# Optimization experiments

Measured on AMD Instinct MI355X. Metric: run time of the kernel, lower is better.

## Reference

```python
import jax, jax.numpy as jnp
import numpy as np

D_MODEL, N_EXPERTS, N_VIEWS, N_TOKENS = 256, 16, 3, 8192

def setup_inputs() -> dict:
    key = jax.random.key(0)
    ks = jax.random.split(key, 10)
    s = 0.05
    return {
        "v0": jax.random.normal(ks[0], (N_TOKENS, D_MODEL), jnp.float32),
        "v1": jax.random.normal(ks[1], (N_TOKENS, D_MODEL), jnp.float32),
        "v2": jax.random.normal(ks[2], (N_TOKENS, D_MODEL), jnp.float32),
        "router_w": jax.random.normal(ks[3], (N_VIEWS, N_EXPERTS, D_MODEL), jnp.float32) * s,
        "expert_keys": jax.random.normal(ks[4], (N_EXPERTS, D_MODEL), jnp.float32) * s,
        "W1": jax.random.normal(ks[5], (N_EXPERTS, D_MODEL, 4 * D_MODEL), jnp.float32) * s,
        "b1": jax.random.normal(ks[6], (N_EXPERTS, 4 * D_MODEL), jnp.float32) * s,
        "W2": jax.random.normal(ks[7], (N_EXPERTS, 4 * D_MODEL, D_MODEL), jnp.float32) * s,
        "b2": jax.random.normal(ks[8], (N_EXPERTS, D_MODEL), jnp.float32) * s,
        "top_k": 4,
    }

def _laplace_gate(v, rw, expert_keys, top_k):
    # -||v - key||^2 expanded: -(|v|^2 + |k|^2 - 2 v.k)   -> [N, E]
    sq = (jnp.sum(v * v, -1, keepdims=True)
          + jnp.sum(expert_keys * expert_keys, -1)[None, :]
          - 2.0 * (v @ expert_keys.T))
    logits = -sq + v @ rw.T                      # router(h), no bias
    topv, topi = jax.lax.top_k(logits, top_k)    # [N, K]
    gate = jax.nn.softmax(topv, axis=-1)         # exp(topv - logsumexp(topv))
    return gate, topi

def reference(v0, v1, v2, router_w, expert_keys, W1, b1, W2, b2, top_k):
    views = [v0, v1, v2]
    E = expert_keys.shape[0]
    N = v0.shape[0]
    fused = jnp.zeros_like(v0)
    rows = jnp.arange(N)[:, None]
    for i, v in enumerate(views):
        gate, idx = _laplace_gate(v, router_w[i], expert_keys, top_k)
        # scatter top-k gates into a dense [N, E] combine matrix
        dense_gate = jnp.zeros((N, E), v.dtype).at[rows, idx].add(gate)
        out = jnp.zeros_like(v)
        for e in range(E):  # fixed small expert loop; each token combined via its gate
            h = jax.nn.gelu(v @ W1[e] + b1[e], approximate=False)
            out = out + dense_gate[:, e:e + 1] * (h @ W2[e] + b2[e])
        fused = fused + out
    return fused
```

## Files before the change

### kernel.cpp

```cpp
#include <hip/hip_runtime.h>
#include <math.h>

#define D_MODEL 256
#define N_EXP   16
#define N_VIEWS 3
#define N_TOK   8192
#define TOPK    4
#define HDIM    1024
#define CH      64
#define NCH     16
#define ROWS    64
#define NGROUP  48
#define NT_STRIPE 2048
#define NT_SPILL  1600
#define NT_TOTAL  (NT_STRIPE + NT_SPILL)
#define REC_ELTS 32768

typedef short s16x8 __attribute__((ext_vector_type(8)));
typedef float f32x4 __attribute__((ext_vector_type(4)));

__device__ __forceinline__ unsigned short f2bf(float x) {
    union { float f; unsigned u; } a; a.f = x;
    unsigned r = a.u + 0x7FFFu + ((a.u >> 16) & 1u);
    return (unsigned short)(r >> 16);
}

__device__ __forceinline__ void dma16(const unsigned short* gp, unsigned short* lp) {
    __builtin_amdgcn_global_load_lds(
        (const __attribute__((address_space(1))) unsigned int*)gp,
        (__attribute__((address_space(3))) unsigned int*)lp, 16, 0, 0);
}

__device__ __forceinline__ void dma_half(const unsigned short* gsrc, unsigned short* ldst,
                                         int wave, int lane) {
    #pragma unroll
    for (int i = 0; i < 4; i++) {
        int blk = wave * 4 + i;
        dma16(gsrc + ((size_t)blk * 64 + lane) * 8, ldst + blk * 512);
    }
}

__global__ __launch_bounds__(256) void wfrag_kernel(const float* __restrict__ W1,
                                                    const float* __restrict__ W2,
                                                    unsigned short* __restrict__ Wf) {
    int c = blockIdx.x, e = blockIdx.y;
    unsigned short* dst = Wf + (size_t)(e * NCH + c) * REC_ELTS;
    if (blockIdx.z == 0) {
        const float* src = W1 + (size_t)e * 256 * 1024;
        #pragma unroll
        for (int i = 0; i < 8; i++) {
            int idx = threadIdx.x + i * 256;
            int lane = idx & 63, nt = (idx >> 6) & 3, ks = idx >> 8;
            int ncol = c * 64 + nt * 16 + (lane & 15);
            int kbase = ks * 32 + (lane >> 4) * 8;
            s16x8 o;
            #pragma unroll
            for (int j = 0; j < 8; j++) o[j] = (short)f2bf(src[(size_t)(kbase + j) * 1024 + ncol]);
            *(s16x8*)(dst + (size_t)idx * 8) = o;
        }
    } else {
        const float* src = W2 + (size_t)e * 1024 * 256;
        dst += 16384;
        #pragma unroll
        for (int i = 0; i < 8; i++) {
            int idx = threadIdx.x + i * 256;
            int lane = idx & 63, ntile = (idx >> 6) & 15, ks2 = idx >> 10;
            int n = ntile * 16 + (lane & 15);
            int kbase = c * 64 + ks2 * 32 + (lane >> 4) * 8;
            s16x8 o;
            #pragma unroll
            for (int j = 0; j < 8; j++) o[j] = (short)f2bf(src[(size_t)(kbase + j) * 256 + n]);
            *(s16x8*)(dst + (size_t)idx * 8) = o;
        }
    }
}

__global__ __launch_bounds__(256) void route_kernel(
    const float* __restrict__ v0, const float* __restrict__ v1, const float* __restrict__ v2,
    const float* __restrict__ rw, const float* __restrict__ keys,
    unsigned short* __restrict__ Xbf,
    int* __restrict__ gidx, float* __restrict__ ggate, int* __restrict__ counts)
{
    __shared__ __align__(16) float cwS[N_EXP * D_MODEL];
    __shared__ float knS[N_EXP];
    __shared__ int lcnt[N_EXP];
    int view = blockIdx.y;
    const float* src = view == 0 ? v0 : (view == 1 ? v1 : v2);
    for (int i = threadIdx.x; i < N_EXP * D_MODEL; i += 256)
        cwS[i] = rw[view * N_EXP * D_MODEL + i] + 2.0f * keys[i];
    if (threadIdx.x < N_EXP) {
        const float4* kp = (const float4*)(keys + threadIdx.x * D_MODEL);
        float s = 0.f;
        for (int d = 0; d < 64; d++) { float4 k = kp[d]; s += k.x*k.x + k.y*k.y + k.z*k.z + k.w*k.w; }
        knS[threadIdx.x] = s; lcnt[threadIdx.x] = 0;
    }
    __syncthreads();

    int wave = threadIdx.x >> 6, lane = threadIdx.x & 63;
    for (int t = 0; t < 16; t++) {
        int token = blockIdx.x * 64 + wave * 16 + t;
        float4 v = ((const float4*)(src + (size_t)token * D_MODEL))[lane];
        ushort4 xo; xo.x = f2bf(v.x); xo.y = f2bf(v.y); xo.z = f2bf(v.z); xo.w = f2bf(v.w);
        ((ushort4*)(Xbf + ((size_t)view * N_TOK + token) * D_MODEL))[lane] = xo;
        float lg[N_EXP];
        #pragma unroll
        for (int e = 0; e < N_EXP; e++) {
            float4 w = *(const float4*)&cwS[e * D_MODEL + lane * 4];
            float p = v.x * w.x + v.y * w.y + v.z * w.z + v.w * w.w;
            #pragma unroll
            for (int s = 32; s > 0; s >>= 1) p += __shfl_xor(p, s, 64);
            lg[e] = p - knS[e];
        }
        int idxs[TOPK]; float vals[TOPK];
        #pragma unroll
        for (int k = 0; k < TOPK; k++) {
            float best = -1e30f; int bi = 0;
            #pragma unroll
            for (int e = 0; e < N_EXP; e++)
                if (lg[e] > best) { best = lg[e]; bi = e; }
            idxs[k] = bi; vals[k] = best;
            #pragma unroll
            for (int e = 0; e < N_EXP; e++)
                lg[e] = (e == bi) ? -1e30f : lg[e];
        }
        float m = vals[0], s = 0.f, ex[TOPK];
        #pragma unroll
        for (int k = 0; k < TOPK; k++) { ex[k] = __expf(vals[k] - m); s += ex[k]; }
        float inv = 1.0f / s;
        if (lane == 0) {
            size_t t4 = ((size_t)view * N_TOK + token) * TOPK;
            int4 gi; gi.x = idxs[0]; gi.y = idxs[1]; gi.z = idxs[2]; gi.w = idxs[3];
            *(int4*)&gidx[t4] = gi;
            float4 gv; gv.x = ex[0]*inv; gv.y = ex[1]*inv; gv.z = ex[2]*inv; gv.w = ex[3]*inv;
            *(float4*)&ggate[t4] = gv;
            atomicAdd(&lcnt[idxs[0]], 1); atomicAdd(&lcnt[idxs[1]], 1);
            atomicAdd(&lcnt[idxs[2]], 1); atomicAdd(&lcnt[idxs[3]], 1);
        }
    }
    __syncthreads();
    if (threadIdx.x < N_EXP && lcnt[threadIdx.x])
        atomicAdd(&counts[view * N_EXP + threadIdx.x], lcnt[threadIdx.x]);
}

__global__ void scan_kernel(const int* __restrict__ counts, int* __restrict__ offs,
                            int* __restrict__ cursor, int* __restrict__ tiles,
                            int* __restrict__ spillCnt) {
    __shared__ int ntS[NGROUP];
    int t = threadIdx.x;
    if (t == 0) spillCnt[0] = 0;
    if (t < NGROUP) ntS[t] = (counts[t] + ROWS - 1) / ROWS;
    for (int s = t; s < NT_TOTAL; s += 64) tiles[s] = -1;
    __syncthreads();
    if (t <= NGROUP) {
        int acc = 0;
        for (int g = 0; g < t && g < NGROUP; g++) acc += counts[g];
        if (t < NGROUP) { offs[t] = acc; cursor[t] = acc; }
        else offs[NGROUP] = acc;
    }
    if (t < NGROUP) {
        int x = (t & 15) >> 1;
        int kstart = 0;
        for (int g2 = 0; g2 < t; g2++)
            if (((g2 & 15) >> 1) == x) kstart += ntS[g2];
        int nt = ntS[t];
        for (int i = 0; i < nt; i++) {
            int k = kstart + i, rec = (t << 16) | i;
            if (k < NT_STRIPE / 8) tiles[x + 8 * k] = rec;
            else {
                int sp = atomicAdd(spillCnt, 1);
                if (sp < NT_SPILL) tiles[NT_STRIPE + sp] = rec;
            }
        }
    }
}

__global__ __launch_bounds__(256) void fill_kernel(const int* __restrict__ gidx,
                                                   const float* __restrict__ ggate,
                                                   int* __restrict__ cursor,
                                                   int* __restrict__ rowTok,
                                                   float* __restrict__ rowGate) {
    __shared__ int lc[N_EXP], lbase[N_EXP];
    int view = blockIdx.y;
    int token = blockIdx.x * 256 + threadIdx.x;
    if (threadIdx.x < N_EXP) lc[threadIdx.x] = 0;
    __syncthreads();
    size_t t4 = ((size_t)view * N_TOK + token) * TOPK;
    int4 e4 = *(const int4*)&gidx[t4];
    float4 g4 = *(const float4*)&ggate[t4];
    int e[4] = { e4.x, e4.y, e4.z, e4.w };
    float gg[4] = { g4.x, g4.y, g4.z, g4.w };
    int lp[4];
    #pragma unroll
    for (int k = 0; k < TOPK; k++) lp[k] = atomicAdd(&lc[e[k]], 1);
    __syncthreads();
    if (threadIdx.x < N_EXP)
        lbase[threadIdx.x] = lc[threadIdx.x] ? atomicAdd(&cursor[view * N_EXP + threadIdx.x], lc[threadIdx.x]) : 0;
    __syncthreads();
    #pragma unroll
    for (int k = 0; k < TOPK; k++) {
        int pos = lbase[e[k]] + lp[k];
        rowTok[pos] = token;
        rowGate[pos] = gg[k];
    }
}

__global__ __launch_bounds__(512, 4) void ffn_kernel(
    const unsigned short* __restrict__ Xbf, const unsigned short* __restrict__ Wf,
    const float* __restrict__ b1, const float* __restrict__ b2,
    const int* __restrict__ offs, const int* __restrict__ tiles,
    const int* __restrict__ rowTok, const float* __restrict__ rowGate,
    float* __restrict__ out)
{
    __shared__ __align__(16) unsigned short Wbuf[REC_ELTS];
    __shared__ __align__(16) unsigned short Hc[ROWS * CH];
    __shared__ int   tokS[ROWS];
    __shared__ float gateS[ROWS];

    int rec = tiles[blockIdx.x];
    if (rec < 0) return;
    int g = rec >> 16, view = g >> 4, e = g & 15;
    int base = offs[g];
    int L = offs[g + 1] - base;
    int r0 = (rec & 0xffff) * ROWS;

    int tid = threadIdx.x;
    int wave = tid >> 6, lane = tid & 63, lmod = lane & 15, quad = lane >> 4;

    const unsigned short* wchunk = Wf + (size_t)e * NCH * REC_ELTS;
    dma_half(wchunk, Wbuf, wave, lane);

    if (tid < ROWS) {
        int gr = r0 + tid; bool ok = gr < L;
        tokS[tid]  = ok ? rowTok[base + gr] : -1;
        gateS[tid] = ok ? rowGate[base + gr] : 0.f;
    }

    int mt1 = wave & 3, nh = wave >> 2;
    int ms  = wave & 1, ns = wave >> 1;

    __syncthreads();

    s16x8 areg[8];
    {
        int token = tokS[mt1 * 16 + lmod];
        if (token < 0) token = 0;
        const unsigned short* xp = Xbf + ((size_t)view * N_TOK + token) * D_MODEL;
        #pragma unroll
        for (int ks = 0; ks < 8; ks++)
            areg[ks] = *(const s16x8*)(xp + ks * 32 + quad * 8);
    }
    dma_half(wchunk + 16384, Wbuf + 16384, wave, lane);

    f32x4 acc2[2][4];
    #pragma unroll
    for (int i = 0; i < 2; i++)
        #pragma unroll
        for (int j = 0; j < 4; j++) acc2[i][j] = (f32x4){0.f, 0.f, 0.f, 0.f};

    for (int c = 0; c < NCH; c++) {
        f32x4 acc1[2];
        acc1[0] = (f32x4){0.f, 0.f, 0.f, 0.f};
        acc1[1] = (f32x4){0.f, 0.f, 0.f, 0.f};
        #pragma unroll
        for (int ks = 0; ks < 8; ks++) {
            #pragma unroll
            for (int nt = 0; nt < 2; nt++) {
                s16x8 b = *(const s16x8*)&Wbuf[((ks * 4 + nh * 2 + nt) * 64 + lane) * 8];
                acc1[nt] = __builtin_amdgcn_mfma_f32_16x16x32_bf16(areg[ks], b, acc1[nt], 0, 0, 0);
            }
        }
        #pragma unroll
        for (int nt = 0; nt < 2; nt++) {
            float bb = b1[e * HDIM + c * CH + (nh * 2 + nt) * 16 + lmod];
            int qa = nt * 2 + (lmod >> 3);
            int baseo = ((mt1 * 2 + nh) * 64 + qa * 16 + quad * 4) * 8 + (lmod & 7);
            #pragma unroll
            for (int r = 0; r < 4; r++) {
                float h = acc1[nt][r] + bb;
                float u = h * (0.7978845608f + 0.0356774081f * h * h);
                float ex2 = __expf(2.f * u);
                float tn = 1.f - 2.f * __builtin_amdgcn_rcpf(1.f + ex2);
                Hc[baseo + r * 8] = f2bf(0.5f * h * (1.f + tn));
            }
        }
        __syncthreads();
        if (c < NCH - 1)
            dma_half(wchunk + (size_t)(c + 1) * REC_ELTS, Wbuf, wave, lane);
        #pragma unroll
        for (int ks2 = 0; ks2 < 2; ks2++) {
            s16x8 afr[2];
            #pragma unroll
            for (int mt = 0; mt < 2; mt++)
                afr[mt] = *(const s16x8*)&Hc[(((ms * 2 + mt) * 2 + ks2) * 64 + lane) * 8];
            #pragma unroll
            for (int nt = 0; nt < 4; nt++) {
                s16x8 b = *(const s16x8*)&Wbuf[16384 + ((ks2 * 16 + ns * 4 + nt) * 64 + lane) * 8];
                #pragma unroll
                for (int mt = 0; mt < 2; mt++)
                    acc2[mt][nt] = __builtin_amdgcn_mfma_f32_16x16x32_bf16(
                        afr[mt], b, acc2[mt][nt], 0, 0, 0);
            }
        }
        __syncthreads();
        if (c < NCH - 1)
            dma_half(wchunk + (size_t)(c + 1) * REC_ELTS + 16384, Wbuf + 16384, wave, lane);
    }

    #pragma unroll
    for (int nt = 0; nt < 4; nt++) {
        int col = (ns * 4 + nt) * 16 + lmod;
        float b2v = b2[e * D_MODEL + col];
        #pragma unroll
        for (int mt = 0; mt < 2; mt++) {
            #pragma unroll
            for (int r = 0; r < 4; r++) {
                int rloc = (ms * 2 + mt) * 16 + quad * 4 + r;
                if (r0 + rloc < L) {
                    atomicAdd(&out[(size_t)tokS[rloc] * D_MODEL + col],
                              gateS[rloc] * (acc2[mt][nt][r] + b2v));
                }
            }
        }
    }
}

extern "C" void kernel_launch(void* const* d_in, const int* in_sizes, int n_in,
                              void* d_out, int out_size, void* d_ws, size_t ws_size,
                              hipStream_t stream)
{
    const float* v0   = (const float*)d_in[0];
    const float* v1   = (const float*)d_in[1];
    const float* v2   = (const float*)d_in[2];
    const float* rw   = (const float*)d_in[3];
    const float* keys = (const float*)d_in[4];
    const float* W1   = (const float*)d_in[5];
    const float* b1   = (const float*)d_in[6];
    const float* W2   = (const float*)d_in[7];
    const float* b2   = (const float*)d_in[8];
    float* out = (float*)d_out;

    char* p = (char*)d_ws;
    unsigned short* Xbf = (unsigned short*)p; p += (size_t)N_VIEWS * N_TOK * D_MODEL * 2;
    unsigned short* Wf  = (unsigned short*)p; p += (size_t)N_EXP * NCH * REC_ELTS * 2;
    int*   counts = (int*)p;   p += 256;
    int*   offs   = (int*)p;   p += 256;
    int*   cursor = (int*)p;   p += 256;
    int*   spill  = (int*)p;   p += 256;
    int*   tiles  = (int*)p;   p += NT_TOTAL * 4 + 64;
    int*   gidx   = (int*)p;   p += (size_t)N_VIEWS * N_TOK * TOPK * 4;
    float* ggate  = (float*)p; p += (size_t)N_VIEWS * N_TOK * TOPK * 4;
    int*   rowTok = (int*)p;   p += (size_t)N_VIEWS * N_TOK * TOPK * 4;
    float* rowGate= (float*)p; p += (size_t)N_VIEWS * N_TOK * TOPK * 4;

    hipMemsetAsync(counts, 0, NGROUP * sizeof(int), stream);
    hipMemsetAsync(out, 0, (size_t)out_size * sizeof(float), stream);

    wfrag_kernel<<<dim3(NCH, N_EXP, 2), 256, 0, stream>>>(W1, W2, Wf);
    route_kernel<<<dim3(N_TOK / 64, N_VIEWS), 256, 0, stream>>>(v0, v1, v2, rw, keys, Xbf,
                                                                gidx, ggate, counts);
    scan_kernel<<<1, 64, 0, stream>>>(counts, offs, cursor, tiles, spill);
    fill_kernel<<<dim3(N_TOK / 256, N_VIEWS), 256, 0, stream>>>(gidx, ggate, cursor,
                                                                rowTok, rowGate);
    ffn_kernel<<<dim3(NT_TOTAL), 512, 0, stream>>>(Xbf, Wf, b1, b2, offs, tiles,
                                                   rowTok, rowGate, out);
}
```

Measured before the change: 393.6 us.

## Warp-specialize FFN into GEMM1/GEMM2 wave groups with 32x32 MFMA and double-buffered H

Splits the FFN block's eight waves into two groups: four waves compute the first GEMM plus GELU for chunk c, while the other four run the second GEMM on chunk c-1 from a double-buffered H tile. Both GEMMs switch from 16x16x32 to 32x32x16 bf16 MFMA, and the weight fragment layout in wfrag_kernel is rewritten to match. The X operand and the output accumulator share one register array, and the spill tile count is reduced. The aim is to overlap the two GEMM phases and cut LDS fragment traffic per MFMA, at the cost of half the waves per phase and higher register pressure.

Measured after the change: 439.4 us. +11.6%, slower.

```diff
diff --git a/kernel.cpp b/kernel.cpp
--- a/kernel.cpp
+++ b/kernel.cpp
@@ -12,12 +12,13 @@
 #define ROWS    64
 #define NGROUP  48
 #define NT_STRIPE 2048
-#define NT_SPILL  1600
+#define NT_SPILL  512
 #define NT_TOTAL  (NT_STRIPE + NT_SPILL)
 #define REC_ELTS 32768
 
 typedef short s16x8 __attribute__((ext_vector_type(8)));
 typedef float f32x4 __attribute__((ext_vector_type(4)));
+typedef float f32x16 __attribute__((ext_vector_type(16)));
 
 __device__ __forceinline__ unsigned short f2bf(float x) {
     union { float f; unsigned u; } a; a.f = x;
@@ -50,9 +51,9 @@
         #pragma unroll
         for (int i = 0; i < 8; i++) {
             int idx = threadIdx.x + i * 256;
-            int lane = idx & 63, nt = (idx >> 6) & 3, ks = idx >> 8;
-            int ncol = c * 64 + nt * 16 + (lane & 15);
-            int kbase = ks * 32 + (lane >> 4) * 8;
+            int lane = idx & 63, nh = (idx >> 6) & 1, kt = idx >> 7;
+            int ncol = c * 64 + nh * 32 + (lane & 31);
+            int kbase = kt * 16 + (lane >> 5) * 8;
             s16x8 o;
             #pragma unroll
             for (int j = 0; j < 8; j++) o[j] = (short)f2bf(src[(size_t)(kbase + j) * 1024 + ncol]);
@@ -64,9 +65,9 @@
         #pragma unroll
         for (int i = 0; i < 8; i++) {
             int idx = threadIdx.x + i * 256;
-            int lane = idx & 63, ntile = (idx >> 6) & 15, ks2 = idx >> 10;
-            int n = ntile * 16 + (lane & 15);
-            int kbase = c * 64 + ks2 * 32 + (lane >> 4) * 8;
+            int lane = idx & 63, nt = (idx >> 6) & 7, kt2 = idx >> 9;
+            int n = nt * 32 + (lane & 31);
+            int kbase = c * 64 + kt2 * 16 + (lane >> 5) * 8;
             s16x8 o;
             #pragma unroll
             for (int j = 0; j < 8; j++) o[j] = (short)f2bf(src[(size_t)(kbase + j) * 256 + n]);
@@ -211,10 +212,9 @@
     const int* __restrict__ rowTok, const float* __restrict__ rowGate,
     float* __restrict__ out)
 {
-    __shared__ __align__(16) unsigned short Wbuf[REC_ELTS];
-    __shared__ __align__(16) unsigned short Hc[ROWS * CH];
-    __shared__ int   tokS[ROWS];
-    __shared__ float gateS[ROWS];
+    __shared__ __align__(16) unsigned short W1s[16384];
+    __shared__ __align__(16) unsigned short W2s[16384];
+    __shared__ __align__(16) unsigned short HcS[2][4096];
 
     int rec = tiles[blockIdx.x];
     if (rec < 0) return;
@@ -224,100 +224,104 @@
     int r0 = (rec & 0xffff) * ROWS;
 
     int tid = threadIdx.x;
-    int wave = tid >> 6, lane = tid & 63, lmod = lane & 15, quad = lane >> 4;
+    int wave = tid >> 6, lane = tid & 63;
+    bool isG1 = wave < 4;
+    int mt = wave & 1, nh = (wave >> 1) & 1;
+    int u = wave & 3, ms = u & 1, ng = u >> 1;
 
     const unsigned short* wchunk = Wf + (size_t)e * NCH * REC_ELTS;
-    dma_half(wchunk, Wbuf, wave, lane);
-
-    if (tid < ROWS) {
-        int gr = r0 + tid; bool ok = gr < L;
-        tokS[tid]  = ok ? rowTok[base + gr] : -1;
-        gateS[tid] = ok ? rowGate[base + gr] : 0.f;
-    }
-
-    int mt1 = wave & 3, nh = wave >> 2;
-    int ms  = wave & 1, ns = wave >> 1;
-
-    __syncthreads();
-
-    s16x8 areg[8];
-    {
-        int token = tokS[mt1 * 16 + lmod];
-        if (token < 0) token = 0;
+    dma_half(wchunk, W1s, wave, lane);
+
+    f32x16 zz;
+    #pragma unroll
+    for (int i = 0; i < 16; i++) zz[i] = 0.f;
+
+    f32x16 st[4];
+    if (isG1) {
+        int gr = r0 + mt * 32 + (lane & 31);
+        int token = (gr < L) ? rowTok[base + gr] : 0;
         const unsigned short* xp = Xbf + ((size_t)view * N_TOK + token) * D_MODEL;
-        #pragma unroll
-        for (int ks = 0; ks < 8; ks++)
-            areg[ks] = *(const s16x8*)(xp + ks * 32 + quad * 8);
-    }
-    dma_half(wchunk + 16384, Wbuf + 16384, wave, lane);
-
-    f32x4 acc2[2][4];
-    #pragma unroll
-    for (int i = 0; i < 2; i++)
-        #pragma unroll
-        for (int j = 0; j < 4; j++) acc2[i][j] = (f32x4){0.f, 0.f, 0.f, 0.f};
-
-    for (int c = 0; c < NCH; c++) {
-        f32x4 acc1[2];
-        acc1[0] = (f32x4){0.f, 0.f, 0.f, 0.f};
-        acc1[1] = (f32x4){0.f, 0.f, 0.f, 0.f};
-        #pragma unroll
-        for (int ks = 0; ks < 8; ks++) {
-            #pragma unroll
-            for (int nt = 0; nt < 2; nt++) {
-                s16x8 b = *(const s16x8*)&Wbuf[((ks * 4 + nh * 2 + nt) * 64 + lane) * 8];
-                acc1[nt] = __builtin_amdgcn_mfma_f32_16x16x32_bf16(areg[ks], b, acc1[nt], 0, 0, 0);
+        int h = lane >> 5;
+        #pragma unroll
+        for (int kt = 0; kt < 16; kt++) {
+            float4 x = *(const float4*)(xp + kt * 16 + h * 8);
+            st[kt >> 2][(kt & 3) * 4 + 0] = x.x;
+            st[kt >> 2][(kt & 3) * 4 + 1] = x.y;
+            st[kt >> 2][(kt & 3) * 4 + 2] = x.z;
+            st[kt >> 2][(kt & 3) * 4 + 3] = x.w;
+        }
+    } else {
+        #pragma unroll
+        for (int i = 0; i < 4; i++) st[i] = zz;
+    }
+    __syncthreads();
+
+    for (int c = 0; c <= NCH; c++) {
+        if (isG1) {
+            if (c < NCH) {
+                f32x16 a0 = zz, a1 = zz;
+                #pragma unroll
+                for (int kt = 0; kt < 16; kt += 2) {
+                    float4 t0 = { st[kt >> 2][(kt & 3) * 4], st[kt >> 2][(kt & 3) * 4 + 1],
+                                  st[kt >> 2][(kt & 3) * 4 + 2], st[kt >> 2][(kt & 3) * 4 + 3] };
+                    s16x8 af0 = __builtin_bit_cast(s16x8, t0);
+                    s16x8 b0 = *(const s16x8*)&W1s[((kt * 2 + nh) * 64 + lane) * 8];
+                    a0 = __builtin_amdgcn_mfma_f32_32x32x16_bf16(af0, b0, a0, 0, 0, 0);
+                    int k1 = kt + 1;
+                    float4 t1 = { st[k1 >> 2][(k1 & 3) * 4], st[k1 >> 2][(k1 & 3) * 4 + 1],
+                                  st[k1 >> 2][(k1 & 3) * 4 + 2], st[k1 >> 2][(k1 & 3) * 4 + 3] };
+                    s16x8 af1 = __builtin_bit_cast(s16x8, t1);
+                    s16x8 b1f = *(const s16x8*)&W1s[((k1 * 2 + nh) * 64 + lane) * 8];
+                    a1 = __builtin_amdgcn_mfma_f32_32x32x16_bf16(af1, b1f, a1, 0, 0, 0);
+                }
+                float bb = b1[e * HDIM + c * CH + nh * 32 + (lane & 31)];
+                unsigned short* hdst = &HcS[c & 1][((mt * 2 + nh) * 16) * 64 + lane];
+                #pragma unroll
+                for (int r = 0; r < 16; r++) {
+                    float hv = a0[r] + a1[r] + bb;
+                    float uu = hv * (0.7978845608f + 0.0356774081f * hv * hv);
+                    float ex2 = __expf(2.f * uu);
+                    float tn = 1.f - 2.f * __builtin_amdgcn_rcpf(1.f + ex2);
+                    hdst[r * 64] = f2bf(0.5f * hv * (1.f + tn));
+                }
             }
-        }
-        #pragma unroll
-        for (int nt = 0; nt < 2; nt++) {
-            float bb = b1[e * HDIM + c * CH + (nh * 2 + nt) * 16 + lmod];
-            int qa = nt * 2 + (lmod >> 3);
-            int baseo = ((mt1 * 2 + nh) * 64 + qa * 16 + quad * 4) * 8 + (lmod & 7);
-            #pragma unroll
-            for (int r = 0; r < 4; r++) {
-                float h = acc1[nt][r] + bb;
-                float u = h * (0.7978845608f + 0.0356774081f * h * h);
-                float ex2 = __expf(2.f * u);
-                float tn = 1.f - 2.f * __builtin_amdgcn_rcpf(1.f + ex2);
-                Hc[baseo + r * 8] = f2bf(0.5f * h * (1.f + tn));
+        } else {
+            if (c > 0) {
+                int row = lane & 31, h = lane >> 5;
+                int r_ = (row & 3) + 4 * (row >> 3);
+                int w5 = (row >> 2) & 1;
+                const unsigned short* hsrc = &HcS[(c - 1) & 1][0];
+                #pragma unroll
+                for (int kt2 = 0; kt2 < 4; kt2++) {
+                    s16x8 a = *(const s16x8*)&hsrc[((ms * 2 + (kt2 >> 1)) * 16 + r_) * 64
+                                                   + w5 * 32 + (kt2 & 1) * 16 + h * 8];
+                    #pragma unroll
+                    for (int nt = 0; nt < 4; nt++) {
+                        s16x8 b = *(const s16x8*)&W2s[((kt2 * 8 + ng * 4 + nt) * 64 + lane) * 8];
+                        st[nt] = __builtin_amdgcn_mfma_f32_32x32x16_bf16(a, b, st[nt], 0, 0, 0);
+                    }
+                }
             }
         }
         __syncthreads();
-        if (c < NCH - 1)
-            dma_half(wchunk + (size_t)(c + 1) * REC_ELTS, Wbuf, wave, lane);
-        #pragma unroll
-        for (int ks2 = 0; ks2 < 2; ks2++) {
-            s16x8 afr[2];
-            #pragma unroll
-            for (int mt = 0; mt < 2; mt++)
-                afr[mt] = *(const s16x8*)&Hc[(((ms * 2 + mt) * 2 + ks2) * 64 + lane) * 8];
-            #pragma unroll
-            for (int nt = 0; nt < 4; nt++) {
-                s16x8 b = *(const s16x8*)&Wbuf[16384 + ((ks2 * 16 + ns * 4 + nt) * 64 + lane) * 8];
-                #pragma unroll
-                for (int mt = 0; mt < 2; mt++)
-                    acc2[mt][nt] = __builtin_amdgcn_mfma_f32_16x16x32_bf16(
-                        afr[mt], b, acc2[mt][nt], 0, 0, 0);
-            }
-        }
+        if (c + 1 < NCH) dma_half(wchunk + (size_t)(c + 1) * REC_ELTS, W1s, wave, lane);
+        if (c < NCH)     dma_half(wchunk + (size_t)c * REC_ELTS + 16384, W2s, wave, lane);
         __syncthreads();
-        if (c < NCH - 1)
-            dma_half(wchunk + (size_t)(c + 1) * REC_ELTS + 16384, Wbuf + 16384, wave, lane);
-    }
-
-    #pragma unroll
-    for (int nt = 0; nt < 4; nt++) {
-        int col = (ns * 4 + nt) * 16 + lmod;
-        float b2v = b2[e * D_MODEL + col];
-        #pragma unroll
-        for (int mt = 0; mt < 2; mt++) {
-            #pragma unroll
-            for (int r = 0; r < 4; r++) {
-                int rloc = (ms * 2 + mt) * 16 + quad * 4 + r;
-                if (r0 + rloc < L) {
-                    atomicAdd(&out[(size_t)tokS[rloc] * D_MODEL + col],
-                              gateS[rloc] * (acc2[mt][nt][r] + b2v));
+    }
+
+    if (!isG1) {
+        #pragma unroll
+        for (int nt = 0; nt < 4; nt++) {
+            int col = (ng * 4 + nt) * 32 + (lane & 31);
+            float b2v = b2[e * D_MODEL + col];
+            #pragma unroll
+            for (int r = 0; r < 16; r++) {
+                int rloc = ms * 32 + (r & 3) + 8 * (r >> 2) + 4 * (lane >> 5);
+                int gr = r0 + rloc;
+                if (gr < L) {
+                    int token = rowTok[base + gr];
+                    float gate = rowGate[base + gr];
+                    atomicAdd(&out[(size_t)token * D_MODEL + col], gate * (st[nt][r] + b2v));
                 }
             }
         }
```

## Merge weight prep with routing and remap FFN first-GEMM wave tiling

Applied to the files above, without the earlier changes.

Fuses the weight-fragment conversion and routing kernels into one launch of 896 blocks, so the two independent jobs can run concurrently and one launch is saved. In the FFN kernel, each wave now computes two M-tiles against a single N-tile, so every B fragment read from LDS feeds two MFMAs. This halves LDS traffic for the first GEMM at the cost of more A registers. The spill tile count is also cut from 1600 to 512, which shrinks the grid but risks dropping tiles if the spill capacity is ever exceeded.

Result: slower. 416.0 us (+5.7%).

```diff
diff --git a/kernel.cpp b/kernel.cpp
--- a/kernel.cpp
+++ b/kernel.cpp
@@ -12,7 +12,7 @@
 #define ROWS    64
 #define NGROUP  48
 #define NT_STRIPE 2048
-#define NT_SPILL  1600
+#define NT_SPILL  512
 #define NT_TOTAL  (NT_STRIPE + NT_SPILL)
 #define REC_ELTS 32768
 
@@ -40,51 +40,54 @@
     }
 }
 
-__global__ __launch_bounds__(256) void wfrag_kernel(const float* __restrict__ W1,
-                                                    const float* __restrict__ W2,
-                                                    unsigned short* __restrict__ Wf) {
-    int c = blockIdx.x, e = blockIdx.y;
-    unsigned short* dst = Wf + (size_t)(e * NCH + c) * REC_ELTS;
-    if (blockIdx.z == 0) {
-        const float* src = W1 + (size_t)e * 256 * 1024;
-        #pragma unroll
-        for (int i = 0; i < 8; i++) {
-            int idx = threadIdx.x + i * 256;
-            int lane = idx & 63, nt = (idx >> 6) & 3, ks = idx >> 8;
-            int ncol = c * 64 + nt * 16 + (lane & 15);
-            int kbase = ks * 32 + (lane >> 4) * 8;
-            s16x8 o;
-            #pragma unroll
-            for (int j = 0; j < 8; j++) o[j] = (short)f2bf(src[(size_t)(kbase + j) * 1024 + ncol]);
-            *(s16x8*)(dst + (size_t)idx * 8) = o;
-        }
-    } else {
-        const float* src = W2 + (size_t)e * 1024 * 256;
-        dst += 16384;
-        #pragma unroll
-        for (int i = 0; i < 8; i++) {
-            int idx = threadIdx.x + i * 256;
-            int lane = idx & 63, ntile = (idx >> 6) & 15, ks2 = idx >> 10;
-            int n = ntile * 16 + (lane & 15);
-            int kbase = c * 64 + ks2 * 32 + (lane >> 4) * 8;
-            s16x8 o;
-            #pragma unroll
-            for (int j = 0; j < 8; j++) o[j] = (short)f2bf(src[(size_t)(kbase + j) * 256 + n]);
-            *(s16x8*)(dst + (size_t)idx * 8) = o;
-        }
-    }
-}
-
-__global__ __launch_bounds__(256) void route_kernel(
+__global__ __launch_bounds__(256) void prep_kernel(
     const float* __restrict__ v0, const float* __restrict__ v1, const float* __restrict__ v2,
     const float* __restrict__ rw, const float* __restrict__ keys,
-    unsigned short* __restrict__ Xbf,
+    const float* __restrict__ W1, const float* __restrict__ W2,
+    unsigned short* __restrict__ Wf, unsigned short* __restrict__ Xbf,
     int* __restrict__ gidx, float* __restrict__ ggate, int* __restrict__ counts)
 {
     __shared__ __align__(16) float cwS[N_EXP * D_MODEL];
     __shared__ float knS[N_EXP];
     __shared__ int lcnt[N_EXP];
-    int view = blockIdx.y;
+
+    int bid = blockIdx.x;
+    if (bid < 512) {
+        int c = bid & 15, e = (bid >> 4) & 15, z = bid >> 8;
+        unsigned short* dst = Wf + (size_t)(e * NCH + c) * REC_ELTS;
+        if (z == 0) {
+            const float* src = W1 + (size_t)e * 256 * 1024;
+            #pragma unroll
+            for (int i = 0; i < 8; i++) {
+                int idx = threadIdx.x + i * 256;
+                int lane = idx & 63, nt = (idx >> 6) & 3, ks = idx >> 8;
+                int ncol = c * 64 + nt * 16 + (lane & 15);
+                int kbase = ks * 32 + (lane >> 4) * 8;
+                s16x8 o;
+                #pragma unroll
+                for (int j = 0; j < 8; j++) o[j] = (short)f2bf(src[(size_t)(kbase + j) * 1024 + ncol]);
+                *(s16x8*)(dst + (size_t)idx * 8) = o;
+            }
+        } else {
+            const float* src = W2 + (size_t)e * 1024 * 256;
+            dst += 16384;
+            #pragma unroll
+            for (int i = 0; i < 8; i++) {
+                int idx = threadIdx.x + i * 256;
+                int lane = idx & 63, ntile = (idx >> 6) & 15, ks2 = idx >> 10;
+                int n = ntile * 16 + (lane & 15);
+                int kbase = c * 64 + ks2 * 32 + (lane >> 4) * 8;
+                s16x8 o;
+                #pragma unroll
+                for (int j = 0; j < 8; j++) o[j] = (short)f2bf(src[(size_t)(kbase + j) * 256 + n]);
+                *(s16x8*)(dst + (size_t)idx * 8) = o;
+            }
+        }
+        return;
+    }
+
+    int rb = bid - 512;
+    int view = rb >> 7, xb = rb & 127;
     const float* src = view == 0 ? v0 : (view == 1 ? v1 : v2);
     for (int i = threadIdx.x; i < N_EXP * D_MODEL; i += 256)
         cwS[i] = rw[view * N_EXP * D_MODEL + i] + 2.0f * keys[i];
@@ -98,7 +101,7 @@
 
     int wave = threadIdx.x >> 6, lane = threadIdx.x & 63;
     for (int t = 0; t < 16; t++) {
-        int token = blockIdx.x * 64 + wave * 16 + t;
+        int token = xb * 64 + wave * 16 + t;
         float4 v = ((const float4*)(src + (size_t)token * D_MODEL))[lane];
         ushort4 xo; xo.x = f2bf(v.x); xo.y = f2bf(v.y); xo.z = f2bf(v.z); xo.w = f2bf(v.w);
         ((ushort4*)(Xbf + ((size_t)view * N_TOK + token) * D_MODEL))[lane] = xo;
@@ -235,19 +238,20 @@
         gateS[tid] = ok ? rowGate[base + gr] : 0.f;
     }
 
-    int mt1 = wave & 3, nh = wave >> 2;
-    int ms  = wave & 1, ns = wave >> 1;
-
-    __syncthreads();
-
-    s16x8 areg[8];
-    {
-        int token = tokS[mt1 * 16 + lmod];
+    int mh  = wave & 1, nt1 = wave >> 1;
+    int ms  = wave & 1, ns  = wave >> 1;
+
+    __syncthreads();
+
+    s16x8 areg[2][8];
+    #pragma unroll
+    for (int mt2 = 0; mt2 < 2; mt2++) {
+        int token = tokS[(mh * 2 + mt2) * 16 + lmod];
         if (token < 0) token = 0;
         const unsigned short* xp = Xbf + ((size_t)view * N_TOK + token) * D_MODEL;
         #pragma unroll
         for (int ks = 0; ks < 8; ks++)
-            areg[ks] = *(const s16x8*)(xp + ks * 32 + quad * 8);
+            areg[mt2][ks] = *(const s16x8*)(xp + ks * 32 + quad * 8);
     }
     dma_half(wchunk + 16384, Wbuf + 16384, wave, lane);
 
@@ -263,24 +267,25 @@
         acc1[1] = (f32x4){0.f, 0.f, 0.f, 0.f};
         #pragma unroll
         for (int ks = 0; ks < 8; ks++) {
-            #pragma unroll
-            for (int nt = 0; nt < 2; nt++) {
-                s16x8 b = *(const s16x8*)&Wbuf[((ks * 4 + nh * 2 + nt) * 64 + lane) * 8];
-                acc1[nt] = __builtin_amdgcn_mfma_f32_16x16x32_bf16(areg[ks], b, acc1[nt], 0, 0, 0);
-            }
-        }
-        #pragma unroll
-        for (int nt = 0; nt < 2; nt++) {
-            float bb = b1[e * HDIM + c * CH + (nh * 2 + nt) * 16 + lmod];
-            int qa = nt * 2 + (lmod >> 3);
-            int baseo = ((mt1 * 2 + nh) * 64 + qa * 16 + quad * 4) * 8 + (lmod & 7);
-            #pragma unroll
-            for (int r = 0; r < 4; r++) {
-                float h = acc1[nt][r] + bb;
-                float u = h * (0.7978845608f + 0.0356774081f * h * h);
-                float ex2 = __expf(2.f * u);
-                float tn = 1.f - 2.f * __builtin_amdgcn_rcpf(1.f + ex2);
-                Hc[baseo + r * 8] = f2bf(0.5f * h * (1.f + tn));
+            s16x8 b = *(const s16x8*)&Wbuf[((ks * 4 + nt1) * 64 + lane) * 8];
+            acc1[0] = __builtin_amdgcn_mfma_f32_16x16x32_bf16(areg[0][ks], b, acc1[0], 0, 0, 0);
+            acc1[1] = __builtin_amdgcn_mfma_f32_16x16x32_bf16(areg[1][ks], b, acc1[1], 0, 0, 0);
+        }
+        {
+            float bb = b1[e * HDIM + c * CH + nt1 * 16 + lmod];
+            int kh = nt1 >> 1;
+            int qa = (nt1 & 1) * 2 + (lmod >> 3);
+            #pragma unroll
+            for (int mt2 = 0; mt2 < 2; mt2++) {
+                int baseo = (((mh * 2 + mt2) * 2 + kh) * 64 + qa * 16 + quad * 4) * 8 + (lmod & 7);
+                #pragma unroll
+                for (int r = 0; r < 4; r++) {
+                    float h = acc1[mt2][r] + bb;
+                    float u = h * (0.7978845608f + 0.0356774081f * h * h);
+                    float ex2 = __expf(2.f * u);
+                    float tn = 1.f - 2.f * __builtin_amdgcn_rcpf(1.f + ex2);
+                    Hc[baseo + r * 8] = f2bf(0.5f * h * (1.f + tn));
+                }
             }
         }
         __syncthreads();
@@ -355,9 +360,8 @@
     hipMemsetAsync(counts, 0, NGROUP * sizeof(int), stream);
     hipMemsetAsync(out, 0, (size_t)out_size * sizeof(float), stream);
 
-    wfrag_kernel<<<dim3(NCH, N_EXP, 2), 256, 0, stream>>>(W1, W2, Wf);
-    route_kernel<<<dim3(N_TOK / 64, N_VIEWS), 256, 0, stream>>>(v0, v1, v2, rw, keys, Xbf,
-                                                                gidx, ggate, counts);
+    prep_kernel<<<896, 256, 0, stream>>>(v0, v1, v2, rw, keys, W1, W2,
+                                         Wf, Xbf, gidx, ggate, counts);
     scan_kernel<<<1, 64, 0, stream>>>(counts, offs, cursor, tiles, spill);
     fill_kernel<<<dim3(N_TOK / 256, N_VIEWS), 256, 0, stream>>>(gidx, ggate, cursor,
                                                                 rowTok, rowGate);
```

## Merge weight repacking and routing into one prep kernel with LDS transpose

Applied to the files above, without the earlier changes.

Combines the weight bf16 fragment repacking and the routing kernel into one launch. The first 512 blocks handle the weights and the remaining 384 blocks do routing. The weight repack now reads W1/W2 with coalesced float4 loads into a padded shared-memory tile and transposes from there, replacing strided scalar global reads. It also cuts the spill tile count, which reduces the number of empty FFN blocks launched but risks overflow if spill demand is high.

After: 391.5 us. Within noise of the previous version (-0.5%).

```diff
diff --git a/kernel.cpp b/kernel.cpp
--- a/kernel.cpp
+++ b/kernel.cpp
@@ -12,7 +12,7 @@
 #define ROWS    64
 #define NGROUP  48
 #define NT_STRIPE 2048
-#define NT_SPILL  1600
+#define NT_SPILL  512
 #define NT_TOTAL  (NT_STRIPE + NT_SPILL)
 #define REC_ELTS 32768
 
@@ -40,65 +40,95 @@
     }
 }
 
-__global__ __launch_bounds__(256) void wfrag_kernel(const float* __restrict__ W1,
-                                                    const float* __restrict__ W2,
-                                                    unsigned short* __restrict__ Wf) {
-    int c = blockIdx.x, e = blockIdx.y;
-    unsigned short* dst = Wf + (size_t)(e * NCH + c) * REC_ELTS;
-    if (blockIdx.z == 0) {
-        const float* src = W1 + (size_t)e * 256 * 1024;
-        #pragma unroll
-        for (int i = 0; i < 8; i++) {
-            int idx = threadIdx.x + i * 256;
-            int lane = idx & 63, nt = (idx >> 6) & 3, ks = idx >> 8;
-            int ncol = c * 64 + nt * 16 + (lane & 15);
-            int kbase = ks * 32 + (lane >> 4) * 8;
-            s16x8 o;
-            #pragma unroll
-            for (int j = 0; j < 8; j++) o[j] = (short)f2bf(src[(size_t)(kbase + j) * 1024 + ncol]);
-            *(s16x8*)(dst + (size_t)idx * 8) = o;
-        }
-    } else {
-        const float* src = W2 + (size_t)e * 1024 * 256;
-        dst += 16384;
-        #pragma unroll
-        for (int i = 0; i < 8; i++) {
-            int idx = threadIdx.x + i * 256;
-            int lane = idx & 63, ntile = (idx >> 6) & 15, ks2 = idx >> 10;
-            int n = ntile * 16 + (lane & 15);
-            int kbase = c * 64 + ks2 * 32 + (lane >> 4) * 8;
-            s16x8 o;
-            #pragma unroll
-            for (int j = 0; j < 8; j++) o[j] = (short)f2bf(src[(size_t)(kbase + j) * 256 + n]);
-            *(s16x8*)(dst + (size_t)idx * 8) = o;
-        }
-    }
-}
-
-__global__ __launch_bounds__(256) void route_kernel(
+#define T1_STRIDE 65
+#define T2_STRIDE 257
+
+__global__ __launch_bounds__(256) void prep_kernel(
     const float* __restrict__ v0, const float* __restrict__ v1, const float* __restrict__ v2,
     const float* __restrict__ rw, const float* __restrict__ keys,
-    unsigned short* __restrict__ Xbf,
+    const float* __restrict__ W1, const float* __restrict__ W2,
+    unsigned short* __restrict__ Wf, unsigned short* __restrict__ Xbf,
     int* __restrict__ gidx, float* __restrict__ ggate, int* __restrict__ counts)
 {
-    __shared__ __align__(16) float cwS[N_EXP * D_MODEL];
-    __shared__ float knS[N_EXP];
-    __shared__ int lcnt[N_EXP];
-    int view = blockIdx.y;
+    __shared__ __align__(16) char smem[256 * T1_STRIDE * 4];
+
+    int bid = blockIdx.x;
+    int tid = threadIdx.x;
+    if (bid < 512) {
+        int c = bid & 15, e = (bid >> 4) & 15, z = bid >> 8;
+        unsigned short* dst = Wf + (size_t)(e * NCH + c) * REC_ELTS;
+        if (z == 0) {
+            float* T1 = (float*)smem;
+            const float* src = W1 + (size_t)e * 256 * 1024 + c * 64;
+            #pragma unroll
+            for (int p = 0; p < 16; p++) {
+                int k = p * 16 + (tid >> 4), c4 = (tid & 15) * 4;
+                float4 v = *(const float4*)(src + (size_t)k * 1024 + c4);
+                T1[k * T1_STRIDE + c4]     = v.x;
+                T1[k * T1_STRIDE + c4 + 1] = v.y;
+                T1[k * T1_STRIDE + c4 + 2] = v.z;
+                T1[k * T1_STRIDE + c4 + 3] = v.w;
+            }
+            __syncthreads();
+            #pragma unroll
+            for (int i = 0; i < 8; i++) {
+                int idx = tid + i * 256;
+                int lane = idx & 63, nt = (idx >> 6) & 3, ks = idx >> 8;
+                int nl = nt * 16 + (lane & 15);
+                int kbase = ks * 32 + (lane >> 4) * 8;
+                s16x8 o;
+                #pragma unroll
+                for (int j = 0; j < 8; j++) o[j] = (short)f2bf(T1[(kbase + j) * T1_STRIDE + nl]);
+                *(s16x8*)(dst + (size_t)idx * 8) = o;
+            }
+        } else {
+            float* T2 = (float*)smem;
+            const float* src = W2 + ((size_t)e * 1024 + c * 64) * 256;
+            #pragma unroll
+            for (int p = 0; p < 16; p++) {
+                int k2l = p * 4 + (tid >> 6), c4 = (tid & 63) * 4;
+                float4 v = *(const float4*)(src + (size_t)k2l * 256 + c4);
+                T2[k2l * T2_STRIDE + c4]     = v.x;
+                T2[k2l * T2_STRIDE + c4 + 1] = v.y;
+                T2[k2l * T2_STRIDE + c4 + 2] = v.z;
+                T2[k2l * T2_STRIDE + c4 + 3] = v.w;
+            }
+            __syncthreads();
+            dst += 16384;
+            #pragma unroll
+            for (int i = 0; i < 8; i++) {
+                int idx = tid + i * 256;
+                int lane = idx & 63, ntile = (idx >> 6) & 15, ks2 = idx >> 10;
+                int n = ntile * 16 + (lane & 15);
+                int kbase = ks2 * 32 + (lane >> 4) * 8;
+                s16x8 o;
+                #pragma unroll
+                for (int j = 0; j < 8; j++) o[j] = (short)f2bf(T2[(kbase + j) * T2_STRIDE + n]);
+                *(s16x8*)(dst + (size_t)idx * 8) = o;
+            }
+        }
+        return;
+    }
+
+    float* cwS = (float*)smem;
+    float* knS = (float*)(smem + 16384);
+    int*  lcnt = (int*)(smem + 16384 + 64);
+    int rb = bid - 512;
+    int view = rb >> 7, xb = rb & 127;
     const float* src = view == 0 ? v0 : (view == 1 ? v1 : v2);
-    for (int i = threadIdx.x; i < N_EXP * D_MODEL; i += 256)
+    for (int i = tid; i < N_EXP * D_MODEL; i += 256)
         cwS[i] = rw[view * N_EXP * D_MODEL + i] + 2.0f * keys[i];
-    if (threadIdx.x < N_EXP) {
-        const float4* kp = (const float4*)(keys + threadIdx.x * D_MODEL);
+    if (tid < N_EXP) {
+        const float4* kp = (const float4*)(keys + tid * D_MODEL);
         float s = 0.f;
         for (int d = 0; d < 64; d++) { float4 k = kp[d]; s += k.x*k.x + k.y*k.y + k.z*k.z + k.w*k.w; }
-        knS[threadIdx.x] = s; lcnt[threadIdx.x] = 0;
-    }
-    __syncthreads();
-
-    int wave = threadIdx.x >> 6, lane = threadIdx.x & 63;
+        knS[tid] = s; lcnt[tid] = 0;
+    }
+    __syncthreads();
+
+    int wave = tid >> 6, lane = tid & 63;
     for (int t = 0; t < 16; t++) {
-        int token = blockIdx.x * 64 + wave * 16 + t;
+        int token = xb * 64 + wave * 16 + t;
         float4 v = ((const float4*)(src + (size_t)token * D_MODEL))[lane];
         ushort4 xo; xo.x = f2bf(v.x); xo.y = f2bf(v.y); xo.z = f2bf(v.z); xo.w = f2bf(v.w);
         ((ushort4*)(Xbf + ((size_t)view * N_TOK + token) * D_MODEL))[lane] = xo;
@@ -138,8 +168,8 @@
         }
     }
     __syncthreads();
-    if (threadIdx.x < N_EXP && lcnt[threadIdx.x])
-        atomicAdd(&counts[view * N_EXP + threadIdx.x], lcnt[threadIdx.x]);
+    if (tid < N_EXP && lcnt[tid])
+        atomicAdd(&counts[view * N_EXP + tid], lcnt[tid]);
 }
 
 __global__ void scan_kernel(const int* __restrict__ counts, int* __restrict__ offs,
@@ -355,9 +385,8 @@
     hipMemsetAsync(counts, 0, NGROUP * sizeof(int), stream);
     hipMemsetAsync(out, 0, (size_t)out_size * sizeof(float), stream);
 
-    wfrag_kernel<<<dim3(NCH, N_EXP, 2), 256, 0, stream>>>(W1, W2, Wf);
-    route_kernel<<<dim3(N_TOK / 64, N_VIEWS), 256, 0, stream>>>(v0, v1, v2, rw, keys, Xbf,
-                                                                gidx, ggate, counts);
+    prep_kernel<<<896, 256, 0, stream>>>(v0, v1, v2, rw, keys, W1, W2,
+                                         Wf, Xbf, gidx, ggate, counts);
     scan_kernel<<<1, 64, 0, stream>>>(counts, offs, cursor, tiles, spill);
     fill_kernel<<<dim3(N_TOK / 256, N_VIEWS), 256, 0, stream>>>(gidx, ggate, cursor,
                                                                 rowTok, rowGate);
```
